# Kernel tuning notes

Hardware: AMD Instinct MI355X
Metric: run time of the kernel (lower is better)

The kernel has to match this reference:

```python
import jax, jax.numpy as jnp
import numpy as np

NUM_HEADS = 8
OUT_CHANNELS = 64  # per-head dim


def setup_inputs() -> dict:
    key = jax.random.key(0)
    ks = jax.random.split(key, 8)
    B, N, C = 8, 16384, 256
    HD = NUM_HEADS * OUT_CHANNELS  # 512
    s = 1.0 / np.sqrt(C)
    return {
        "query_input": jax.random.normal(ks[0], (B, N, C), jnp.float32),
        "source_input": jax.random.normal(ks[1], (B, N, C), jnp.float32),
        "Wq_w": jax.random.normal(ks[2], (C, HD), jnp.float32) * s,
        "Wq_b": jax.random.normal(ks[3], (HD,), jnp.float32) * s,
        "Wk_w": jax.random.normal(ks[4], (C, HD), jnp.float32) * s,
        "Wk_b": jax.random.normal(ks[5], (HD,), jnp.float32) * s,
        "Wv_w": jax.random.normal(ks[6], (C, HD), jnp.float32) * s,
        "Wv_b": jax.random.normal(ks[7], (HD,), jnp.float32) * s,
    }


def reference(query_input, source_input, Wq_w, Wq_b, Wk_w, Wk_b, Wv_w, Wv_b):
    B, N, _ = query_input.shape
    L = source_input.shape[1]
    H, D = NUM_HEADS, OUT_CHANNELS

    qs = (query_input @ Wq_w + Wq_b).reshape(B, N, H, D)
    ks = (source_input @ Wk_w + Wk_b).reshape(B, L, H, D)
    vs = (source_input @ Wv_w + Wv_b).reshape(B, L, H, D)

    # L2-normalize queries and keys along feature dim (cosine kernel)
    qs = qs / jnp.linalg.norm(qs, axis=-1, keepdims=True)
    ks = ks / jnp.linalg.norm(ks, axis=-1, keepdims=True)

    Nf = jnp.float32(N)
    # kv aggregation: [B,H,D_k,D_v]
    kvs = jnp.einsum('blhm,blhd->bhmd', ks, vs)
    # numerator: q . kv  +  N * sum_l v_l  (broadcast over n)
    attention_num = jnp.einsum('bnhm,bhmd->bnhd', qs, kvs) \
        + Nf * vs.sum(axis=1, keepdims=True)
    # normalizer: q . sum_l k_l  + N + N
    ks_sum = ks.sum(axis=1)  # [B,H,D]
    attention_normalizer = jnp.einsum('bnhm,bhm->bnh', qs, ks_sum)[..., None] + Nf + Nf

    attn_output = attention_num / attention_normalizer  # [B,N,H,D]
    return attn_output.mean(axis=2)  # mean over heads -> [B,N,D]
```

## Files before the change

### kernel.cpp

```cpp
#include <hip/hip_runtime.h>

#define B_   8
#define N_   16384
#define C_   256
#define H_   8
#define D_   64
#define HD_  512
#define BN_  (B_ * N_)
#define NF   16384.0f

typedef __attribute__((ext_vector_type(8))) short short8;
typedef __attribute__((ext_vector_type(4))) float f32x4;

typedef unsigned short bhalf;

__device__ __forceinline__ bhalf f2bf(float x) {
    union { float f; unsigned u; } v; v.f = x;
    unsigned r = v.u + 0x7fffu + ((v.u >> 16) & 1u);
    return (bhalf)(r >> 16);
}
__device__ __forceinline__ float bf2f(bhalf h) {
    union { unsigned u; float f; } v; v.u = ((unsigned)h) << 16;
    return v.f;
}

__global__ void cast_w_kernel(const float* __restrict__ Wq, const float* __restrict__ Wk,
                              const float* __restrict__ Wv, const float* __restrict__ bq,
                              const float* __restrict__ bk, const float* __restrict__ bv,
                              bhalf* __restrict__ WT, float* __restrict__ biasCat)
{
    int c = blockIdx.x;
    int k = threadIdx.x;
    int sec = c >> 9, cs = c & 511;
    const float* W = (sec == 0) ? Wq : (sec == 1 ? Wk : Wv);
    WT[(size_t)c * C_ + k] = f2bf(W[(size_t)k * HD_ + cs]);
    if (k == 0) {
        const float* bb = (sec == 0) ? bq : (sec == 1 ? bk : bv);
        biasCat[c] = bb[cs];
    }
}

__global__ __launch_bounds__(256) void proj_kernel(
    const float* __restrict__ query, const float* __restrict__ source,
    const bhalf* __restrict__ WT, const float* __restrict__ biasCat,
    bhalf* __restrict__ qn, bhalf* __restrict__ kn, bhalf* __restrict__ vv,
    float* __restrict__ ksum, float* __restrict__ vsum)
{
    const int ct = blockIdx.x;
    const int rt = blockIdx.y;
    const int section = ct >> 2;
    const int sec_col0 = (ct & 3) * 128;
    const int row0 = rt * 128;
    const int b = row0 >> 14;

    const float* Abase = (section == 0 ? query : source) + (size_t)row0 * C_;
    const bhalf* Wbase = WT + (size_t)(section * HD_ + sec_col0) * C_;

    __shared__ bhalf As[128 * 32];
    __shared__ bhalf Bs[128 * 32];

    const int tid  = threadIdx.x;
    const int wave = tid >> 6;
    const int lane = tid & 63;
    const int l15  = lane & 15;
    const int quad = lane >> 4;
    const int wm = (wave >> 1) * 64;
    const int wn = (wave & 1) * 64;

    f32x4 acc[4][4];
#pragma unroll
    for (int i = 0; i < 4; ++i)
#pragma unroll
        for (int j = 0; j < 4; ++j)
            acc[i][j] = (f32x4)(0.0f);

    const int sr = tid >> 1;
    const int sc = (tid & 1) * 16;

    for (int kk = 0; kk < C_; kk += 32) {
        {
            const float* src = Abase + (size_t)sr * C_ + kk + sc;
            float tmp[16];
            *(float4*)&tmp[0]  = *(const float4*)(src + 0);
            *(float4*)&tmp[4]  = *(const float4*)(src + 4);
            *(float4*)&tmp[8]  = *(const float4*)(src + 8);
            *(float4*)&tmp[12] = *(const float4*)(src + 12);
            bhalf* dst = &As[sr * 32 + sc];
#pragma unroll
            for (int e = 0; e < 16; ++e) dst[e] = f2bf(tmp[e]);
        }
        {
            const uint4* s4 = (const uint4*)(Wbase + (size_t)sr * C_ + kk + sc);
            uint4* d4 = (uint4*)&Bs[sr * 32 + sc];
            d4[0] = s4[0]; d4[1] = s4[1];
        }
        __syncthreads();

        short8 af[4], bfr[4];
#pragma unroll
        for (int i = 0; i < 4; ++i)
            af[i] = *(const short8*)&As[(wm + i * 16 + l15) * 32 + quad * 8];
#pragma unroll
        for (int j = 0; j < 4; ++j)
            bfr[j] = *(const short8*)&Bs[(wn + j * 16 + l15) * 32 + quad * 8];
#pragma unroll
        for (int i = 0; i < 4; ++i)
#pragma unroll
            for (int j = 0; j < 4; ++j)
                acc[i][j] = __builtin_amdgcn_mfma_f32_16x16x32_bf16(af[i], bfr[j], acc[i][j], 0, 0, 0);
        __syncthreads();
    }

    float bv4[4];
#pragma unroll
    for (int j = 0; j < 4; ++j)
        bv4[j] = biasCat[section * HD_ + sec_col0 + wn + j * 16 + l15];
#pragma unroll
    for (int i = 0; i < 4; ++i)
#pragma unroll
        for (int j = 0; j < 4; ++j)
#pragma unroll
            for (int r = 0; r < 4; ++r)
                acc[i][j][r] += bv4[j];

    if (section <= 1) {
#pragma unroll
        for (int i = 0; i < 4; ++i)
#pragma unroll
            for (int r = 0; r < 4; ++r) {
                float s = 0.f;
#pragma unroll
                for (int j = 0; j < 4; ++j) s += acc[i][j][r] * acc[i][j][r];
                s += __shfl_xor(s, 1, 64);
                s += __shfl_xor(s, 2, 64);
                s += __shfl_xor(s, 4, 64);
                s += __shfl_xor(s, 8, 64);
                float scl = rsqrtf(s);
#pragma unroll
                for (int j = 0; j < 4; ++j) acc[i][j][r] *= scl;
            }
    }
    if (section >= 1) {
        float* sums = (section == 1) ? ksum : vsum;
#pragma unroll
        for (int j = 0; j < 4; ++j) {
            float cs = 0.f;
#pragma unroll
            for (int i = 0; i < 4; ++i)
#pragma unroll
                for (int r = 0; r < 4; ++r) cs += acc[i][j][r];
            cs += __shfl_xor(cs, 16, 64);
            cs += __shfl_xor(cs, 32, 64);
            if (quad == 0)
                atomicAdd(&sums[b * HD_ + sec_col0 + wn + j * 16 + l15], cs);
        }
    }

    bhalf* outp = (section == 0) ? qn : (section == 1 ? kn : vv);
#pragma unroll
    for (int i = 0; i < 4; ++i)
#pragma unroll
        for (int r = 0; r < 4; ++r) {
            size_t row = (size_t)(row0 + wm + i * 16 + quad * 4 + r);
#pragma unroll
            for (int j = 0; j < 4; ++j)
                outp[row * HD_ + sec_col0 + wn + j * 16 + l15] = f2bf(acc[i][j][r]);
        }
}

__global__ __launch_bounds__(256) void kv_kernel(
    const bhalf* __restrict__ kn, const bhalf* __restrict__ vv,
    float* __restrict__ kvs)
{
    const int bh = blockIdx.x & 63;
    const int ls = blockIdx.x >> 6;
    const int b = bh >> 3, h = bh & 7;
    const int l0blk = ls * 1024;

    __shared__ bhalf Ks[128 * 66];
    __shared__ bhalf Vs[128 * 66];
    __shared__ float kvsL[64 * 64];

    const int tid = threadIdx.x;
    const int wave = tid >> 6, lane = tid & 63;
    const int l15 = lane & 15, quad = lane >> 4;

    for (int i = tid; i < 4096; i += 256) kvsL[i] = 0.f;

    f32x4 acc[4][4];
#pragma unroll
    for (int i = 0; i < 4; ++i)
#pragma unroll
        for (int j = 0; j < 4; ++j)
            acc[i][j] = (f32x4)(0.0f);

    const int srow = tid & 127;
    const int scol = (tid >> 7) * 32;

    for (int ch = 0; ch < 8; ++ch) {
        int l0 = l0blk + ch * 128;
        {
            size_t gbase = ((size_t)(b * N_ + l0 + srow)) * HD_ + h * D_ + scol;
            const uint4* ksrc = (const uint4*)(kn + gbase);
            const uint4* vsrc = (const uint4*)(vv + gbase);
#pragma unroll
            for (int q4 = 0; q4 < 4; ++q4) {
                uint4 kw = ksrc[q4];
                uint4 vw = vsrc[q4];
                unsigned* kd = (unsigned*)&Ks[srow * 66 + scol + q4 * 8];
                unsigned* vd = (unsigned*)&Vs[srow * 66 + scol + q4 * 8];
                kd[0] = kw.x; kd[1] = kw.y; kd[2] = kw.z; kd[3] = kw.w;
                vd[0] = vw.x; vd[1] = vw.y; vd[2] = vw.z; vd[3] = vw.w;
            }
        }
        __syncthreads();

        const int lrow = wave * 32 + quad * 8;
        short8 af[4], bfr[4];
#pragma unroll
        for (int i = 0; i < 4; ++i) {
            short8 t;
#pragma unroll
            for (int jj = 0; jj < 8; ++jj)
                t[jj] = (short)Ks[(lrow + jj) * 66 + i * 16 + l15];
            af[i] = t;
        }
#pragma unroll
        for (int j = 0; j < 4; ++j) {
            short8 t;
#pragma unroll
            for (int jj = 0; jj < 8; ++jj)
                t[jj] = (short)Vs[(lrow + jj) * 66 + j * 16 + l15];
            bfr[j] = t;
        }
#pragma unroll
        for (int i = 0; i < 4; ++i)
#pragma unroll
            for (int j = 0; j < 4; ++j)
                acc[i][j] = __builtin_amdgcn_mfma_f32_16x16x32_bf16(af[i], bfr[j], acc[i][j], 0, 0, 0);
        __syncthreads();
    }

#pragma unroll
    for (int i = 0; i < 4; ++i)
#pragma unroll
        for (int j = 0; j < 4; ++j)
#pragma unroll
            for (int r = 0; r < 4; ++r)
                atomicAdd(&kvsL[(i * 16 + quad * 4 + r) * 64 + j * 16 + l15], acc[i][j][r]);
    __syncthreads();
    float* kvg = kvs + (size_t)bh * 4096;
    for (int i = tid; i < 4096; i += 256) atomicAdd(&kvg[i], kvsL[i]);
}

__global__ void prep_b_kernel(const float* __restrict__ kvs,
                              const float* __restrict__ ksum,
                              bhalf* __restrict__ Btb)
{
    const int bh = blockIdx.x;
    const int b = bh >> 3, h = bh & 7;
    const float* kvg = kvs + (size_t)bh * 4096;
    const float* ksg = ksum + b * HD_ + h * 64;
    bhalf* o = Btb + (size_t)bh * 80 * 64;
    for (int idx = threadIdx.x; idx < 80 * 64; idx += 256) {
        int n = idx >> 6, k = idx & 63;
        float val = (n < 64) ? kvg[k * 64 + n] : (n == 64 ? ksg[k] : 0.0f);
        o[idx] = f2bf(val);
    }
}

__global__ __launch_bounds__(256) void attn_kernel(
    const bhalf* __restrict__ qn, const bhalf* __restrict__ Btb,
    const float* __restrict__ vsum, float* __restrict__ out)
{
    const int tid  = threadIdx.x;
    const int wave = tid >> 6;
    const int lane = tid & 63;
    const int l15  = lane & 15;
    const int quad = lane >> 4;
    const int row0 = blockIdx.x * 128 + wave * 32;
    const int b = row0 >> 14;

    f32x4 outacc[2][4];
#pragma unroll
    for (int i = 0; i < 2; ++i)
#pragma unroll
        for (int j = 0; j < 4; ++j)
            outacc[i][j] = (f32x4)(0.0f);

#pragma unroll
    for (int h = 0; h < 8; ++h) {
        short8 af[2][2];
#pragma unroll
        for (int i = 0; i < 2; ++i)
#pragma unroll
            for (int kk = 0; kk < 2; ++kk)
                af[i][kk] = *(const short8*)(qn +
                    (size_t)(row0 + i * 16 + l15) * HD_ + h * 64 + kk * 32 + quad * 8);

        const bhalf* Bb = Btb + (size_t)(b * 8 + h) * 80 * 64;
        short8 bfr[5][2];
#pragma unroll
        for (int j = 0; j < 5; ++j)
#pragma unroll
            for (int kk = 0; kk < 2; ++kk)
                bfr[j][kk] = *(const short8*)(Bb + (j * 16 + l15) * 64 + kk * 32 + quad * 8);

        f32x4 nacc[2][5];
#pragma unroll
        for (int i = 0; i < 2; ++i)
#pragma unroll
            for (int j = 0; j < 5; ++j)
                nacc[i][j] = (f32x4)(0.0f);
#pragma unroll
        for (int kk = 0; kk < 2; ++kk)
#pragma unroll
            for (int i = 0; i < 2; ++i)
#pragma unroll
                for (int j = 0; j < 5; ++j)
                    nacc[i][j] = __builtin_amdgcn_mfma_f32_16x16x32_bf16(
                        af[i][kk], bfr[j][kk], nacc[i][j], 0, 0, 0);

        float vsv[4];
#pragma unroll
        for (int j = 0; j < 4; ++j)
            vsv[j] = vsum[b * HD_ + h * 64 + j * 16 + l15];

#pragma unroll
        for (int i = 0; i < 2; ++i)
#pragma unroll
            for (int r = 0; r < 4; ++r) {
                float den = __shfl(nacc[i][4][r], quad << 4, 64) + 2.0f * NF;
                float rden = 1.0f / den;
#pragma unroll
                for (int j = 0; j < 4; ++j)
                    outacc[i][j][r] += (nacc[i][j][r] + NF * vsv[j]) * rden;
            }
    }

#pragma unroll
    for (int i = 0; i < 2; ++i)
#pragma unroll
        for (int r = 0; r < 4; ++r) {
            size_t row = (size_t)(row0 + i * 16 + quad * 4 + r);
#pragma unroll
            for (int j = 0; j < 4; ++j)
                out[row * D_ + j * 16 + l15] = outacc[i][j][r] * 0.125f;
        }
}

extern "C" void kernel_launch(void* const* d_in, const int* in_sizes, int n_in,
                              void* d_out, int out_size, void* d_ws, size_t ws_size,
                              hipStream_t stream)
{
    const float* query  = (const float*)d_in[0];
    const float* source = (const float*)d_in[1];
    const float* Wq = (const float*)d_in[2];
    const float* bq = (const float*)d_in[3];
    const float* Wk = (const float*)d_in[4];
    const float* bk = (const float*)d_in[5];
    const float* Wv = (const float*)d_in[6];
    const float* bv = (const float*)d_in[7];

    char* ws = (char*)d_ws;
    bhalf* qn      = (bhalf*)(ws + 0);
    bhalf* kn      = (bhalf*)(ws + 134217728);
    bhalf* vv      = (bhalf*)(ws + 268435456);
    bhalf* WT      = (bhalf*)(ws + 402653184);
    float* biasCat = (float*)(ws + 403439616);
    float* ksum    = (float*)(ws + 403445760);
    float* vsum    = (float*)(ws + 403462144);
    float* kvs     = (float*)(ws + 403478528);
    bhalf* Btb     = (bhalf*)(ws + 404527104);

    hipMemsetAsync(ws + 403445760, 0, 16384 + 16384 + 1048576, stream);

    cast_w_kernel<<<1536, 256, 0, stream>>>(Wq, Wk, Wv, bq, bk, bv, WT, biasCat);
    proj_kernel<<<dim3(12, 1024), 256, 0, stream>>>(query, source, WT, biasCat,
                                                    qn, kn, vv, ksum, vsum);
    kv_kernel<<<1024, 256, 0, stream>>>(kn, vv, kvs);
    prep_b_kernel<<<64, 256, 0, stream>>>(kvs, ksum, Btb);
    attn_kernel<<<1024, 256, 0, stream>>>(qn, Btb, vsum, (float*)d_out);
}
```

Measured before the change: 838.9 us.

## Fuse K/V projection with KV aggregation and Q projection with attention

Merges the K/V projection into the kv aggregation kernel, so normalized K and V tiles stay in shared memory and feed the K^T V MFMAs directly. Likewise, the Q projection moves into the attention kernel, so qn is never written to global memory. This removes the large bf16 intermediates (qn/kn/vv, about 400MB of write-then-read traffic) and two kernel launches. In exchange, the K/V kernel runs only 256 blocks at one block per CU with heavy register use, and weights are read from global memory per block, which may limit occupancy and parallelism.

```diff
diff --git a/kernel.cpp b/kernel.cpp
--- a/kernel.cpp
+++ b/kernel.cpp
@@ -6,8 +6,10 @@
 #define H_   8
 #define D_   64
 #define HD_  512
-#define BN_  (B_ * N_)
 #define NF   16384.0f
+
+#define AP   280
+#define SP   136
 
 typedef __attribute__((ext_vector_type(8))) short short8;
 typedef __attribute__((ext_vector_type(4))) float f32x4;
@@ -40,217 +42,179 @@
     }
 }
 
-__global__ __launch_bounds__(256) void proj_kernel(
-    const float* __restrict__ query, const float* __restrict__ source,
-    const bhalf* __restrict__ WT, const float* __restrict__ biasCat,
-    bhalf* __restrict__ qn, bhalf* __restrict__ kn, bhalf* __restrict__ vv,
-    float* __restrict__ ksum, float* __restrict__ vsum)
+__global__ __launch_bounds__(256, 1) void proj_kv_kernel(
+    const float* __restrict__ source, const bhalf* __restrict__ WT,
+    const float* __restrict__ biasCat, float* __restrict__ ksum,
+    float* __restrict__ vsum, float* __restrict__ kvs)
 {
-    const int ct = blockIdx.x;
-    const int rt = blockIdx.y;
-    const int section = ct >> 2;
-    const int sec_col0 = (ct & 3) * 128;
-    const int row0 = rt * 128;
-    const int b = row0 >> 14;
-
-    const float* Abase = (section == 0 ? query : source) + (size_t)row0 * C_;
-    const bhalf* Wbase = WT + (size_t)(section * HD_ + sec_col0) * C_;
-
-    __shared__ bhalf As[128 * 32];
-    __shared__ bhalf Bs[128 * 32];
+    __shared__ bhalf As[128 * AP];
+    __shared__ bhalf kS[128 * SP];
+    __shared__ bhalf vS[128 * SP];
 
     const int tid  = threadIdx.x;
     const int wave = tid >> 6;
     const int lane = tid & 63;
     const int l15  = lane & 15;
     const int quad = lane >> 4;
-    const int wm = (wave >> 1) * 64;
-    const int wn = (wave & 1) * 64;
-
-    f32x4 acc[4][4];
-#pragma unroll
-    for (int i = 0; i < 4; ++i)
-#pragma unroll
-        for (int j = 0; j < 4; ++j)
-            acc[i][j] = (f32x4)(0.0f);
-
-    const int sr = tid >> 1;
-    const int sc = (tid & 1) * 16;
-
-    for (int kk = 0; kk < C_; kk += 32) {
+    const int wr   = wave >> 1;
+    const int wc   = wave & 1;
+    const int base_row = blockIdx.x * 512;
+    const int b = base_row >> 14;
+    const int mh = wr * 32;
+
+    f32x4 kvacc[4][2][4];
+#pragma unroll
+    for (int hp = 0; hp < 4; ++hp)
+#pragma unroll
+        for (int mi = 0; mi < 2; ++mi)
+#pragma unroll
+            for (int dj = 0; dj < 4; ++dj)
+                kvacc[hp][mi][dj] = (f32x4)(0.0f);
+
+    for (int rt = 0; rt < 4; ++rt) {
+        const int row0 = base_row + rt * 128;
+        __syncthreads();
         {
-            const float* src = Abase + (size_t)sr * C_ + kk + sc;
-            float tmp[16];
-            *(float4*)&tmp[0]  = *(const float4*)(src + 0);
-            *(float4*)&tmp[4]  = *(const float4*)(src + 4);
-            *(float4*)&tmp[8]  = *(const float4*)(src + 8);
-            *(float4*)&tmp[12] = *(const float4*)(src + 12);
-            bhalf* dst = &As[sr * 32 + sc];
-#pragma unroll
-            for (int e = 0; e < 16; ++e) dst[e] = f2bf(tmp[e]);
-        }
-        {
-            const uint4* s4 = (const uint4*)(Wbase + (size_t)sr * C_ + kk + sc);
-            uint4* d4 = (uint4*)&Bs[sr * 32 + sc];
-            d4[0] = s4[0]; d4[1] = s4[1];
+            const int sr = tid >> 1, sco = (tid & 1) * 16;
+            const float* srcp = source + (size_t)(row0 + sr) * C_ + sco;
+#pragma unroll
+            for (int kk = 0; kk < 8; ++kk) {
+                float t[16];
+                *(float4*)&t[0]  = *(const float4*)(srcp + kk * 32 + 0);
+                *(float4*)&t[4]  = *(const float4*)(srcp + kk * 32 + 4);
+                *(float4*)&t[8]  = *(const float4*)(srcp + kk * 32 + 8);
+                *(float4*)&t[12] = *(const float4*)(srcp + kk * 32 + 12);
+                bhalf hh[16];
+#pragma unroll
+                for (int e = 0; e < 16; ++e) hh[e] = f2bf(t[e]);
+                *(uint4*)&As[sr * AP + kk * 32 + sco]     = *(uint4*)&hh[0];
+                *(uint4*)&As[sr * AP + kk * 32 + sco + 8] = *(uint4*)&hh[8];
+            }
         }
         __syncthreads();
 
-        short8 af[4], bfr[4];
-#pragma unroll
-        for (int i = 0; i < 4; ++i)
-            af[i] = *(const short8*)&As[(wm + i * 16 + l15) * 32 + quad * 8];
-#pragma unroll
-        for (int j = 0; j < 4; ++j)
-            bfr[j] = *(const short8*)&Bs[(wn + j * 16 + l15) * 32 + quad * 8];
-#pragma unroll
-        for (int i = 0; i < 4; ++i)
-#pragma unroll
-            for (int j = 0; j < 4; ++j)
-                acc[i][j] = __builtin_amdgcn_mfma_f32_16x16x32_bf16(af[i], bfr[j], acc[i][j], 0, 0, 0);
-        __syncthreads();
-    }
-
-    float bv4[4];
-#pragma unroll
-    for (int j = 0; j < 4; ++j)
-        bv4[j] = biasCat[section * HD_ + sec_col0 + wn + j * 16 + l15];
-#pragma unroll
-    for (int i = 0; i < 4; ++i)
-#pragma unroll
-        for (int j = 0; j < 4; ++j)
-#pragma unroll
-            for (int r = 0; r < 4; ++r)
-                acc[i][j][r] += bv4[j];
-
-    if (section <= 1) {
-#pragma unroll
-        for (int i = 0; i < 4; ++i)
-#pragma unroll
-            for (int r = 0; r < 4; ++r) {
-                float s = 0.f;
-#pragma unroll
-                for (int j = 0; j < 4; ++j) s += acc[i][j][r] * acc[i][j][r];
-                s += __shfl_xor(s, 1, 64);
-                s += __shfl_xor(s, 2, 64);
-                s += __shfl_xor(s, 4, 64);
-                s += __shfl_xor(s, 8, 64);
-                float scl = rsqrtf(s);
-#pragma unroll
-                for (int j = 0; j < 4; ++j) acc[i][j][r] *= scl;
-            }
-    }
-    if (section >= 1) {
-        float* sums = (section == 1) ? ksum : vsum;
-#pragma unroll
-        for (int j = 0; j < 4; ++j) {
-            float cs = 0.f;
-#pragma unroll
-            for (int i = 0; i < 4; ++i)
-#pragma unroll
-                for (int r = 0; r < 4; ++r) cs += acc[i][j][r];
-            cs += __shfl_xor(cs, 16, 64);
-            cs += __shfl_xor(cs, 32, 64);
-            if (quad == 0)
-                atomicAdd(&sums[b * HD_ + sec_col0 + wn + j * 16 + l15], cs);
-        }
-    }
-
-    bhalf* outp = (section == 0) ? qn : (section == 1 ? kn : vv);
-#pragma unroll
-    for (int i = 0; i < 4; ++i)
-#pragma unroll
-        for (int r = 0; r < 4; ++r) {
-            size_t row = (size_t)(row0 + wm + i * 16 + quad * 4 + r);
-#pragma unroll
-            for (int j = 0; j < 4; ++j)
-                outp[row * HD_ + sec_col0 + wn + j * 16 + l15] = f2bf(acc[i][j][r]);
-        }
-}
-
-__global__ __launch_bounds__(256) void kv_kernel(
-    const bhalf* __restrict__ kn, const bhalf* __restrict__ vv,
-    float* __restrict__ kvs)
-{
-    const int bh = blockIdx.x & 63;
-    const int ls = blockIdx.x >> 6;
-    const int b = bh >> 3, h = bh & 7;
-    const int l0blk = ls * 1024;
-
-    __shared__ bhalf Ks[128 * 66];
-    __shared__ bhalf Vs[128 * 66];
-    __shared__ float kvsL[64 * 64];
-
-    const int tid = threadIdx.x;
-    const int wave = tid >> 6, lane = tid & 63;
-    const int l15 = lane & 15, quad = lane >> 4;
-
-    for (int i = tid; i < 4096; i += 256) kvsL[i] = 0.f;
-
-    f32x4 acc[4][4];
-#pragma unroll
-    for (int i = 0; i < 4; ++i)
-#pragma unroll
-        for (int j = 0; j < 4; ++j)
-            acc[i][j] = (f32x4)(0.0f);
-
-    const int srow = tid & 127;
-    const int scol = (tid >> 7) * 32;
-
-    for (int ch = 0; ch < 8; ++ch) {
-        int l0 = l0blk + ch * 128;
-        {
-            size_t gbase = ((size_t)(b * N_ + l0 + srow)) * HD_ + h * D_ + scol;
-            const uint4* ksrc = (const uint4*)(kn + gbase);
-            const uint4* vsrc = (const uint4*)(vv + gbase);
-#pragma unroll
-            for (int q4 = 0; q4 < 4; ++q4) {
-                uint4 kw = ksrc[q4];
-                uint4 vw = vsrc[q4];
-                unsigned* kd = (unsigned*)&Ks[srow * 66 + scol + q4 * 8];
-                unsigned* vd = (unsigned*)&Vs[srow * 66 + scol + q4 * 8];
-                kd[0] = kw.x; kd[1] = kw.y; kd[2] = kw.z; kd[3] = kw.w;
-                vd[0] = vw.x; vd[1] = vw.y; vd[2] = vw.z; vd[3] = vw.w;
-            }
-        }
-        __syncthreads();
-
-        const int lrow = wave * 32 + quad * 8;
-        short8 af[4], bfr[4];
-#pragma unroll
-        for (int i = 0; i < 4; ++i) {
-            short8 t;
-#pragma unroll
-            for (int jj = 0; jj < 8; ++jj)
-                t[jj] = (short)Ks[(lrow + jj) * 66 + i * 16 + l15];
-            af[i] = t;
-        }
-#pragma unroll
-        for (int j = 0; j < 4; ++j) {
-            short8 t;
-#pragma unroll
-            for (int jj = 0; jj < 8; ++jj)
-                t[jj] = (short)Vs[(lrow + jj) * 66 + j * 16 + l15];
-            bfr[j] = t;
-        }
-#pragma unroll
-        for (int i = 0; i < 4; ++i)
-#pragma unroll
-            for (int j = 0; j < 4; ++j)
-                acc[i][j] = __builtin_amdgcn_mfma_f32_16x16x32_bf16(af[i], bfr[j], acc[i][j], 0, 0, 0);
-        __syncthreads();
-    }
-
-#pragma unroll
-    for (int i = 0; i < 4; ++i)
-#pragma unroll
-        for (int j = 0; j < 4; ++j)
-#pragma unroll
-            for (int r = 0; r < 4; ++r)
-                atomicAdd(&kvsL[(i * 16 + quad * 4 + r) * 64 + j * 16 + l15], acc[i][j][r]);
-    __syncthreads();
-    float* kvg = kvs + (size_t)bh * 4096;
-    for (int i = tid; i < 4096; i += 256) atomicAdd(&kvg[i], kvsL[i]);
+        for (int hp = 0; hp < 4; ++hp) {
+            f32x4 acck[4][4], accv[4][4];
+#pragma unroll
+            for (int i = 0; i < 4; ++i)
+#pragma unroll
+                for (int j = 0; j < 4; ++j) {
+                    acck[i][j] = (f32x4)(0.0f);
+                    accv[i][j] = (f32x4)(0.0f);
+                }
+            const int colb = hp * 128 + wc * 64;
+            const bhalf* WK = WT + (size_t)(HD_ + colb) * C_;
+            const bhalf* WV = WT + (size_t)(2 * HD_ + colb) * C_;
+#pragma unroll
+            for (int ks = 0; ks < 8; ++ks) {
+                short8 af[4];
+#pragma unroll
+                for (int i = 0; i < 4; ++i)
+                    af[i] = *(const short8*)&As[(wr * 64 + i * 16 + l15) * AP + ks * 32 + quad * 8];
+                short8 bk8[4], bv8[4];
+#pragma unroll
+                for (int j = 0; j < 4; ++j) {
+                    bk8[j] = *(const short8*)(WK + (size_t)(j * 16 + l15) * C_ + ks * 32 + quad * 8);
+                    bv8[j] = *(const short8*)(WV + (size_t)(j * 16 + l15) * C_ + ks * 32 + quad * 8);
+                }
+#pragma unroll
+                for (int i = 0; i < 4; ++i)
+#pragma unroll
+                    for (int j = 0; j < 4; ++j) {
+                        acck[i][j] = __builtin_amdgcn_mfma_f32_16x16x32_bf16(af[i], bk8[j], acck[i][j], 0, 0, 0);
+                        accv[i][j] = __builtin_amdgcn_mfma_f32_16x16x32_bf16(af[i], bv8[j], accv[i][j], 0, 0, 0);
+                    }
+            }
+#pragma unroll
+            for (int j = 0; j < 4; ++j) {
+                float bkj = biasCat[HD_ + colb + j * 16 + l15];
+                float bvj = biasCat[2 * HD_ + colb + j * 16 + l15];
+#pragma unroll
+                for (int i = 0; i < 4; ++i)
+#pragma unroll
+                    for (int r = 0; r < 4; ++r) {
+                        acck[i][j][r] += bkj;
+                        accv[i][j][r] += bvj;
+                    }
+            }
+#pragma unroll
+            for (int i = 0; i < 4; ++i)
+#pragma unroll
+                for (int r = 0; r < 4; ++r) {
+                    float s = 0.f;
+#pragma unroll
+                    for (int j = 0; j < 4; ++j) s += acck[i][j][r] * acck[i][j][r];
+                    s += __shfl_xor(s, 1, 64);
+                    s += __shfl_xor(s, 2, 64);
+                    s += __shfl_xor(s, 4, 64);
+                    s += __shfl_xor(s, 8, 64);
+                    float scl = rsqrtf(s);
+#pragma unroll
+                    for (int j = 0; j < 4; ++j) acck[i][j][r] *= scl;
+                }
+#pragma unroll
+            for (int j = 0; j < 4; ++j) {
+                float csk = 0.f, csv = 0.f;
+#pragma unroll
+                for (int i = 0; i < 4; ++i)
+#pragma unroll
+                    for (int r = 0; r < 4; ++r) { csk += acck[i][j][r]; csv += accv[i][j][r]; }
+                csk += __shfl_xor(csk, 16, 64);
+                csk += __shfl_xor(csk, 32, 64);
+                csv += __shfl_xor(csv, 16, 64);
+                csv += __shfl_xor(csv, 32, 64);
+                if (quad == 0) {
+                    atomicAdd(&ksum[b * HD_ + colb + j * 16 + l15], csk);
+                    atomicAdd(&vsum[b * HD_ + colb + j * 16 + l15], csv);
+                }
+            }
+#pragma unroll
+            for (int i = 0; i < 4; ++i)
+#pragma unroll
+                for (int j = 0; j < 4; ++j) {
+                    uint2 uk, uv;
+                    uk.x = (unsigned)f2bf(acck[i][j][0]) | ((unsigned)f2bf(acck[i][j][1]) << 16);
+                    uk.y = (unsigned)f2bf(acck[i][j][2]) | ((unsigned)f2bf(acck[i][j][3]) << 16);
+                    uv.x = (unsigned)f2bf(accv[i][j][0]) | ((unsigned)f2bf(accv[i][j][1]) << 16);
+                    uv.y = (unsigned)f2bf(accv[i][j][2]) | ((unsigned)f2bf(accv[i][j][3]) << 16);
+                    int feat = wc * 64 + j * 16 + l15;
+                    int lofs = wr * 64 + i * 16 + quad * 4;
+                    *(uint2*)&kS[feat * SP + lofs] = uk;
+                    *(uint2*)&vS[feat * SP + lofs] = uv;
+                }
+            __syncthreads();
+#pragma unroll
+            for (int k2 = 0; k2 < 4; ++k2) {
+                short8 ak[2];
+#pragma unroll
+                for (int mi = 0; mi < 2; ++mi)
+                    ak[mi] = *(const short8*)&kS[(wc * 64 + mh + mi * 16 + l15) * SP + k2 * 32 + quad * 8];
+                short8 bv2[4];
+#pragma unroll
+                for (int dj = 0; dj < 4; ++dj)
+                    bv2[dj] = *(const short8*)&vS[(wc * 64 + dj * 16 + l15) * SP + k2 * 32 + quad * 8];
+#pragma unroll
+                for (int mi = 0; mi < 2; ++mi)
+#pragma unroll
+                    for (int dj = 0; dj < 4; ++dj)
+                        kvacc[hp][mi][dj] = __builtin_amdgcn_mfma_f32_16x16x32_bf16(
+                            ak[mi], bv2[dj], kvacc[hp][mi][dj], 0, 0, 0);
+            }
+            __syncthreads();
+        }
+    }
+#pragma unroll
+    for (int hp = 0; hp < 4; ++hp) {
+        float* kvg = kvs + (size_t)(b * 8 + hp * 2 + wc) * 4096;
+#pragma unroll
+        for (int mi = 0; mi < 2; ++mi)
+#pragma unroll
+            for (int dj = 0; dj < 4; ++dj)
+#pragma unroll
+                for (int r = 0; r < 4; ++r)
+                    atomicAdd(&kvg[(mh + mi * 16 + quad * 4 + r) * 64 + dj * 16 + l15],
+                              kvacc[hp][mi][dj][r]);
+    }
 }
 
 __global__ void prep_b_kernel(const float* __restrict__ kvs,
@@ -269,17 +233,42 @@
     }
 }
 
-__global__ __launch_bounds__(256) void attn_kernel(
-    const bhalf* __restrict__ qn, const bhalf* __restrict__ Btb,
+__global__ __launch_bounds__(256, 1) void qattn_kernel(
+    const float* __restrict__ query, const bhalf* __restrict__ WT,
+    const float* __restrict__ biasCat, const bhalf* __restrict__ Btb,
     const float* __restrict__ vsum, float* __restrict__ out)
 {
+    __shared__ bhalf As[128 * AP];
+    __shared__ bhalf qS[128 * SP];
+
     const int tid  = threadIdx.x;
     const int wave = tid >> 6;
     const int lane = tid & 63;
     const int l15  = lane & 15;
     const int quad = lane >> 4;
-    const int row0 = blockIdx.x * 128 + wave * 32;
+    const int wr   = wave >> 1;
+    const int wc   = wave & 1;
+    const int row0 = blockIdx.x * 128;
     const int b = row0 >> 14;
+
+    {
+        const int sr = tid >> 1, sco = (tid & 1) * 16;
+        const float* srcp = query + (size_t)(row0 + sr) * C_ + sco;
+#pragma unroll
+        for (int kk = 0; kk < 8; ++kk) {
+            float t[16];
+            *(float4*)&t[0]  = *(const float4*)(srcp + kk * 32 + 0);
+            *(float4*)&t[4]  = *(const float4*)(srcp + kk * 32 + 4);
+            *(float4*)&t[8]  = *(const float4*)(srcp + kk * 32 + 8);
+            *(float4*)&t[12] = *(const float4*)(srcp + kk * 32 + 12);
+            bhalf hh[16];
+#pragma unroll
+            for (int e = 0; e < 16; ++e) hh[e] = f2bf(t[e]);
+            *(uint4*)&As[sr * AP + kk * 32 + sco]     = *(uint4*)&hh[0];
+            *(uint4*)&As[sr * AP + kk * 32 + sco + 8] = *(uint4*)&hh[8];
+        }
+    }
+    __syncthreads();
 
     f32x4 outacc[2][4];
 #pragma unroll
@@ -288,61 +277,118 @@
         for (int j = 0; j < 4; ++j)
             outacc[i][j] = (f32x4)(0.0f);
 
-#pragma unroll
-    for (int h = 0; h < 8; ++h) {
-        short8 af[2][2];
-#pragma unroll
-        for (int i = 0; i < 2; ++i)
+    for (int ch = 0; ch < 4; ++ch) {
+        f32x4 acc[4][4];
+#pragma unroll
+        for (int i = 0; i < 4; ++i)
+#pragma unroll
+            for (int j = 0; j < 4; ++j)
+                acc[i][j] = (f32x4)(0.0f);
+        const int colb = ch * 128 + wc * 64;
+        const bhalf* WQ = WT + (size_t)colb * C_;
+#pragma unroll
+        for (int ks = 0; ks < 8; ++ks) {
+            short8 af[4];
+#pragma unroll
+            for (int i = 0; i < 4; ++i)
+                af[i] = *(const short8*)&As[(wr * 64 + i * 16 + l15) * AP + ks * 32 + quad * 8];
+            short8 bq8[4];
+#pragma unroll
+            for (int j = 0; j < 4; ++j)
+                bq8[j] = *(const short8*)(WQ + (size_t)(j * 16 + l15) * C_ + ks * 32 + quad * 8);
+#pragma unroll
+            for (int i = 0; i < 4; ++i)
+#pragma unroll
+                for (int j = 0; j < 4; ++j)
+                    acc[i][j] = __builtin_amdgcn_mfma_f32_16x16x32_bf16(af[i], bq8[j], acc[i][j], 0, 0, 0);
+        }
+#pragma unroll
+        for (int j = 0; j < 4; ++j) {
+            float bj = biasCat[colb + j * 16 + l15];
+#pragma unroll
+            for (int i = 0; i < 4; ++i)
+#pragma unroll
+                for (int r = 0; r < 4; ++r) acc[i][j][r] += bj;
+        }
+#pragma unroll
+        for (int i = 0; i < 4; ++i)
+#pragma unroll
+            for (int r = 0; r < 4; ++r) {
+                float s = 0.f;
+#pragma unroll
+                for (int j = 0; j < 4; ++j) s += acc[i][j][r] * acc[i][j][r];
+                s += __shfl_xor(s, 1, 64);
+                s += __shfl_xor(s, 2, 64);
+                s += __shfl_xor(s, 4, 64);
+                s += __shfl_xor(s, 8, 64);
+                float scl = rsqrtf(s);
+#pragma unroll
+                for (int j = 0; j < 4; ++j) acc[i][j][r] *= scl;
+            }
+#pragma unroll
+        for (int i = 0; i < 4; ++i)
+#pragma unroll
+            for (int j = 0; j < 4; ++j)
+#pragma unroll
+                for (int r = 0; r < 4; ++r)
+                    qS[(wr * 64 + i * 16 + quad * 4 + r) * SP + wc * 64 + j * 16 + l15]
+                        = f2bf(acc[i][j][r]);
+        __syncthreads();
+
+#pragma unroll
+        for (int hl = 0; hl < 2; ++hl) {
+            const int h = ch * 2 + hl;
+            const bhalf* Bb = Btb + (size_t)(b * 8 + h) * 80 * 64;
+            short8 af2[2][2];
+#pragma unroll
+            for (int i = 0; i < 2; ++i)
+#pragma unroll
+                for (int kk = 0; kk < 2; ++kk)
+                    af2[i][kk] = *(const short8*)&qS[(wave * 32 + i * 16 + l15) * SP
+                                                     + hl * 64 + kk * 32 + quad * 8];
+            short8 bfr[5][2];
+#pragma unroll
+            for (int j = 0; j < 5; ++j)
+#pragma unroll
+                for (int kk = 0; kk < 2; ++kk)
+                    bfr[j][kk] = *(const short8*)(Bb + (j * 16 + l15) * 64 + kk * 32 + quad * 8);
+            f32x4 nacc[2][5];
+#pragma unroll
+            for (int i = 0; i < 2; ++i)
+#pragma unroll
+                for (int j = 0; j < 5; ++j)
+                    nacc[i][j] = (f32x4)(0.0f);
 #pragma unroll
             for (int kk = 0; kk < 2; ++kk)
-                af[i][kk] = *(const short8*)(qn +
-                    (size_t)(row0 + i * 16 + l15) * HD_ + h * 64 + kk * 32 + quad * 8);
-
-        const bhalf* Bb = Btb + (size_t)(b * 8 + h) * 80 * 64;
-        short8 bfr[5][2];
-#pragma unroll
-        for (int j = 0; j < 5; ++j)
-#pragma unroll
-            for (int kk = 0; kk < 2; ++kk)
-                bfr[j][kk] = *(const short8*)(Bb + (j * 16 + l15) * 64 + kk * 32 + quad * 8);
-
-        f32x4 nacc[2][5];
-#pragma unroll
-        for (int i = 0; i < 2; ++i)
-#pragma unroll
-            for (int j = 0; j < 5; ++j)
-                nacc[i][j] = (f32x4)(0.0f);
-#pragma unroll
-        for (int kk = 0; kk < 2; ++kk)
+#pragma unroll
+                for (int i = 0; i < 2; ++i)
+#pragma unroll
+                    for (int j = 0; j < 5; ++j)
+                        nacc[i][j] = __builtin_amdgcn_mfma_f32_16x16x32_bf16(
+                            af2[i][kk], bfr[j][kk], nacc[i][j], 0, 0, 0);
+            float vsv[4];
+#pragma unroll
+            for (int j = 0; j < 4; ++j)
+                vsv[j] = vsum[b * HD_ + h * 64 + j * 16 + l15];
 #pragma unroll
             for (int i = 0; i < 2; ++i)
 #pragma unroll
-                for (int j = 0; j < 5; ++j)
-                    nacc[i][j] = __builtin_amdgcn_mfma_f32_16x16x32_bf16(
-                        af[i][kk], bfr[j][kk], nacc[i][j], 0, 0, 0);
-
-        float vsv[4];
-#pragma unroll
-        for (int j = 0; j < 4; ++j)
-            vsv[j] = vsum[b * HD_ + h * 64 + j * 16 + l15];
-
-#pragma unroll
-        for (int i = 0; i < 2; ++i)
-#pragma unroll
-            for (int r = 0; r < 4; ++r) {
-                float den = __shfl(nacc[i][4][r], quad << 4, 64) + 2.0f * NF;
-                float rden = 1.0f / den;
-#pragma unroll
-                for (int j = 0; j < 4; ++j)
-                    outacc[i][j][r] += (nacc[i][j][r] + NF * vsv[j]) * rden;
-            }
+                for (int r = 0; r < 4; ++r) {
+                    float den = __shfl(nacc[i][4][r], quad << 4, 64) + 2.0f * NF;
+                    float rden = 1.0f / den;
+#pragma unroll
+                    for (int j = 0; j < 4; ++j)
+                        outacc[i][j][r] += (nacc[i][j][r] + NF * vsv[j]) * rden;
+                }
+        }
+        __syncthreads();
     }
 
 #pragma unroll
     for (int i = 0; i < 2; ++i)
 #pragma unroll
         for (int r = 0; r < 4; ++r) {
-            size_t row = (size_t)(row0 + i * 16 + quad * 4 + r);
+            size_t row = (size_t)(row0 + wave * 32 + i * 16 + quad * 4 + r);
 #pragma unroll
             for (int j = 0; j < 4; ++j)
                 out[row * D_ + j * 16 + l15] = outacc[i][j][r] * 0.125f;
@@ -363,22 +409,17 @@
     const float* bv = (const float*)d_in[7];
 
     char* ws = (char*)d_ws;
-    bhalf* qn      = (bhalf*)(ws + 0);
-    bhalf* kn      = (bhalf*)(ws + 134217728);
-    bhalf* vv      = (bhalf*)(ws + 268435456);
-    bhalf* WT      = (bhalf*)(ws + 402653184);
-    float* biasCat = (float*)(ws + 403439616);
-    float* ksum    = (float*)(ws + 403445760);
-    float* vsum    = (float*)(ws + 403462144);
-    float* kvs     = (float*)(ws + 403478528);
-    bhalf* Btb     = (bhalf*)(ws + 404527104);
-
-    hipMemsetAsync(ws + 403445760, 0, 16384 + 16384 + 1048576, stream);
+    bhalf* WT      = (bhalf*)(ws + 0);
+    float* biasCat = (float*)(ws + 786432);
+    float* ksum    = (float*)(ws + 792576);
+    float* vsum    = (float*)(ws + 808960);
+    float* kvs     = (float*)(ws + 825344);
+    bhalf* Btb     = (bhalf*)(ws + 1873920);
+
+    hipMemsetAsync(ws + 792576, 0, 16384 + 16384 + 1048576, stream);
 
     cast_w_kernel<<<1536, 256, 0, stream>>>(Wq, Wk, Wv, bq, bk, bv, WT, biasCat);
-    proj_kernel<<<dim3(12, 1024), 256, 0, stream>>>(query, source, WT, biasCat,
-                                                    qn, kn, vv, ksum, vsum);
-    kv_kernel<<<1024, 256, 0, stream>>>(kn, vv, kvs);
+    proj_kv_kernel<<<256, 256, 0, stream>>>(source, WT, biasCat, ksum, vsum, kvs);
     prep_b_kernel<<<64, 256, 0, stream>>>(kvs, ksum, Btb);
-    attn_kernel<<<1024, 256, 0, stream>>>(qn, Btb, vsum, (float*)d_out);
-}
+    qattn_kernel<<<1024, 256, 0, stream>>>(query, WT, biasCat, Btb, vsum, (float*)d_out);
+}
```

Measured after the change: 694.6 us. 17.2% less time.
